# Performance work log

Measured on AMD Instinct MI355X. Metric: run time of the kernel, lower is better.

## Reference

```python
import jax, jax.numpy as jnp
import numpy as np

NUM_POINTS = 32
POINT_DIM = 4
HIDDEN_DIM = 256
BATCH = 8192


def setup_inputs() -> dict:
    key = jax.random.key(0)
    k1, k2, k3 = jax.random.split(key, 3)
    path_data = jax.random.normal(k1, (BATCH, NUM_POINTS * POINT_DIM), dtype=jnp.float32)
    # per-step Linear(point_dim+hidden_dim -> hidden_dim); torch Linear weight layout [out, in]
    fan_in = POINT_DIM + HIDDEN_DIM
    scale = 1.0 / np.sqrt(fan_in)
    W = jax.random.uniform(k2, (NUM_POINTS, HIDDEN_DIM, fan_in), dtype=jnp.float32, minval=-scale, maxval=scale)
    b = jax.random.uniform(k3, (NUM_POINTS, HIDDEN_DIM), dtype=jnp.float32, minval=-scale, maxval=scale)
    return {"path_data": path_data, "W": W, "b": b}


def reference(path_data, W, b):
    P, H = W.shape[0], W.shape[1]
    B = path_data.shape[0]
    pd = W.shape[2] - H
    # chunks: [P, B, point_dim]
    chunks = path_data.reshape(B, P, pd).transpose(1, 0, 2)

    def step(h, xs):
        wp, Wi, bi = xs
        # concat order matches torch: (curr_hidden, current_wp)
        combined = jnp.concatenate([h, wp], axis=1)  # [B, H+pd]
        h_new = jax.nn.relu(combined @ Wi.T + bi)    # [B, H]
        return h_new, h_new

    h0 = jnp.zeros((B, H), dtype=path_data.dtype)
    _, feats = jax.lax.scan(step, h0, (chunks, W, b))  # feats: [P, B, H]
    return feats.transpose(1, 0, 2).reshape(B, P * H)
```

## Files before the change

### kernel.cpp

```cpp
#include <hip/hip_runtime.h>

typedef __attribute__((ext_vector_type(8))) short bf16x8;
typedef __attribute__((ext_vector_type(16))) float f32x16;

#define NPTS 32
#define HID 256
#define FANIN 260
#define NKB 17
#define OUTSTRIDE 8192

__device__ __forceinline__ unsigned short f2bf(float f) {
  unsigned u = __builtin_bit_cast(unsigned, f);
  u += 0x7fffu + ((u >> 16) & 1u);
  return (unsigned short)(u >> 16);
}

__global__ __launch_bounds__(256) void prep_kernel(
    const float* __restrict__ W, const float* __restrict__ bias,
    bf16x8* __restrict__ pack) {
  int tid = blockIdx.x * 256 + threadIdx.x;
  int lane = tid & 63;
  int kb = (tid >> 6) % NKB;
  int rest = (tid >> 6) / NKB;
  int ct = rest & 7;
  int p = rest >> 3;
  if (p >= NPTS) return;
  int n = ct * 32 + (lane & 31);
  int g = lane >> 5;
  const float* wrow = W + (size_t)(p * HID + n) * FANIN;
  unsigned short e[8];
  if (kb < 16) {
    int k0 = kb * 16 + g * 8;
#pragma unroll
    for (int i = 0; i < 8; ++i) e[i] = f2bf(wrow[k0 + i]);
  } else {
#pragma unroll
    for (int i = 0; i < 8; ++i) e[i] = 0;
    if (g == 0) {
      e[0] = f2bf(wrow[256]);
      e[1] = f2bf(wrow[257]);
      e[2] = f2bf(wrow[258]);
      e[3] = f2bf(wrow[259]);
      e[4] = f2bf(bias[p * HID + n]);
    }
  }
  bf16x8 v;
#pragma unroll
  for (int i = 0; i < 8; ++i) v[i] = (short)e[i];
  pack[tid] = v;
}

__global__ __launch_bounds__(512, 1) void enc_kernel(
    const float* __restrict__ path, const bf16x8* __restrict__ pack,
    float* __restrict__ out) {
  __shared__ __align__(16) char lds[32768];
  const int tid = threadIdx.x;
  const int lane = tid & 63;
  const int w = tid >> 6;
  const int col = lane & 31;
  const int g = lane >> 5;
  const int b0 = blockIdx.x * 32;

  {
    int4 z = make_int4(0, 0, 0, 0);
    *reinterpret_cast<int4*>(lds + tid * 32) = z;
    *reinterpret_cast<int4*>(lds + tid * 32 + 16) = z;
  }
  __syncthreads();

  const float4* prow =
      reinterpret_cast<const float4*>(path + (size_t)(b0 + col) * 128);

  int cur = 0;
  const int swz = col << 4;

  for (int p = 0; p < NPTS; ++p) {
    const bf16x8* Bp = pack + (size_t)((p * 8 + w) * NKB) * 64 + lane;

    f32x16 acc0, acc1;
#pragma unroll
    for (int i = 0; i < 16; ++i) { acc0[i] = 0.0f; acc1[i] = 0.0f; }

    float4 px = prow[p];
    bf16x8 ax;
#pragma unroll
    for (int i = 0; i < 8; ++i) ax[i] = 0;
    if (g == 0) {
      ax[0] = (short)f2bf(px.x);
      ax[1] = (short)f2bf(px.y);
      ax[2] = (short)f2bf(px.z);
      ax[3] = (short)f2bf(px.w);
      ax[4] = (short)0x3F80;
    }

    const char* hb = lds + cur * 16384;
#pragma unroll
    for (int kb = 0; kb < 16; ++kb) {
      bf16x8 a = *reinterpret_cast<const bf16x8*>(
          hb + col * 512 + ((kb * 32 + g * 16) ^ swz));
      bf16x8 bb = Bp[kb * 64];
      if (kb & 1)
        acc1 = __builtin_amdgcn_mfma_f32_32x32x16_bf16(a, bb, acc1, 0, 0, 0);
      else
        acc0 = __builtin_amdgcn_mfma_f32_32x32x16_bf16(a, bb, acc0, 0, 0, 0);
    }
    acc0 = __builtin_amdgcn_mfma_f32_32x32x16_bf16(ax, Bp[16 * 64], acc0, 0, 0, 0);

    char* hn = lds + (cur ^ 1) * 16384;
    float* outp = out + (size_t)b0 * OUTSTRIDE + p * 256 + w * 32 + col;
#pragma unroll
    for (int r = 0; r < 16; ++r) {
      int rr = (r & 3) + 8 * (r >> 2) + 4 * g;
      float v = fmaxf(acc0[r] + acc1[r], 0.0f);
      outp[(size_t)rr * OUTSTRIDE] = v;
      *reinterpret_cast<unsigned short*>(
          hn + rr * 512 + (((w * 32 + col) * 2) ^ (rr << 4))) = f2bf(v);
    }
    __syncthreads();
    cur ^= 1;
  }
}

extern "C" void kernel_launch(void* const* d_in, const int* in_sizes, int n_in,
                              void* d_out, int out_size, void* d_ws,
                              size_t ws_size, hipStream_t stream) {
  const float* path = (const float*)d_in[0];
  const float* W = (const float*)d_in[1];
  const float* bias = (const float*)d_in[2];
  float* out = (float*)d_out;
  bf16x8* pack = (bf16x8*)d_ws;

  prep_kernel<<<1088, 256, 0, stream>>>(W, bias, pack);
  enc_kernel<<<256, 512, 0, stream>>>(path, pack, out);
}
```

Measured before the change: 100.7 us.

## Prefetch next step's weights into registers and use lighter barriers in encoder

Loads all weight fragments for the next recurrence step into a second register set (ping-pong BA/BB) while the current step's MFMAs run, and also prefetches the next point's input. It replaces __syncthreads with an LDS-only waitcnt plus s_barrier so global stores need not drain at each step. Output stores become nontemporal, and the launch bound is raised to two blocks per CU. The risks are higher register pressure from two full weight sets, possible spills under the new occupancy hint, and one redundant prefetch of step 0 on the last iteration.

```diff
diff --git a/kernel.cpp b/kernel.cpp
--- a/kernel.cpp
+++ b/kernel.cpp
@@ -50,7 +50,7 @@
   pack[tid] = v;
 }
 
-__global__ __launch_bounds__(512, 1) void enc_kernel(
+__global__ __launch_bounds__(512, 2) void enc_kernel(
     const float* __restrict__ path, const bf16x8* __restrict__ pack,
     float* __restrict__ out) {
   __shared__ __align__(16) char lds[32768];
@@ -66,59 +66,78 @@
     *reinterpret_cast<int4*>(lds + tid * 32) = z;
     *reinterpret_cast<int4*>(lds + tid * 32 + 16) = z;
   }
-  __syncthreads();
 
   const float4* prow =
       reinterpret_cast<const float4*>(path + (size_t)(b0 + col) * 128);
+  float* outbase = out + (size_t)b0 * OUTSTRIDE;
+  const int swz = col << 4;
+  int cur = 0;
 
-  int cur = 0;
-  const int swz = col << 4;
+  bf16x8 BA[NKB], BB[NKB];
+  float4 pxA, pxB;
+  {
+    const bf16x8* Bp0 = pack + (size_t)w * NKB * 64 + lane;
+#pragma unroll
+    for (int kb = 0; kb < NKB; ++kb) BA[kb] = Bp0[kb * 64];
+    pxA = prow[0];
+  }
+  __syncthreads();
 
-  for (int p = 0; p < NPTS; ++p) {
-    const bf16x8* Bp = pack + (size_t)((p * 8 + w) * NKB) * 64 + lane;
+#define STEP(P, BC, BN, PX, PXN, PNEXT)                                       \
+  {                                                                           \
+    const int p_ = (P);                                                       \
+    const bf16x8* Bnp =                                                       \
+        pack + ((size_t)((PNEXT) * 8 + w) * NKB) * 64 + lane;                 \
+    f32x16 acc0, acc1;                                                        \
+    _Pragma("unroll") for (int i = 0; i < 16; ++i) {                          \
+      acc0[i] = 0.0f;                                                         \
+      acc1[i] = 0.0f;                                                         \
+    }                                                                         \
+    bf16x8 ax;                                                                \
+    _Pragma("unroll") for (int i = 0; i < 8; ++i) ax[i] = 0;                  \
+    if (g == 0) {                                                             \
+      ax[0] = (short)f2bf((PX).x);                                            \
+      ax[1] = (short)f2bf((PX).y);                                            \
+      ax[2] = (short)f2bf((PX).z);                                            \
+      ax[3] = (short)f2bf((PX).w);                                            \
+      ax[4] = (short)0x3F80;                \
+    }                                                                         \
+    const char* hb = lds + cur * 16384;                                       \
+    _Pragma("unroll") for (int kb = 0; kb < 16; ++kb) {                       \
+      bf16x8 a = *reinterpret_cast<const bf16x8*>(                            \
+          hb + col * 512 + ((kb * 32 + g * 16) ^ swz));                       \
+      if (kb & 1)                                                             \
+        acc1 = __builtin_amdgcn_mfma_f32_32x32x16_bf16(a, (BC)[kb], acc1,     \
+                                                       0, 0, 0);              \
+      else                                                                    \
+        acc0 = __builtin_amdgcn_mfma_f32_32x32x16_bf16(a, (BC)[kb], acc0,     \
+                                                       0, 0, 0);              \
+      (BN)[kb] = Bnp[kb * 64]; \
+    }                                                                         \
+    acc0 = __builtin_amdgcn_mfma_f32_32x32x16_bf16(ax, (BC)[16], acc0,        \
+                                                   0, 0, 0);                  \
+    (BN)[16] = Bnp[16 * 64];                                                  \
+    (PXN) = prow[(PNEXT)];                                                    \
+    char* hn = lds + (cur ^ 1) * 16384;                                       \
+    float* outp = outbase + p_ * 256 + w * 32 + col;                          \
+    _Pragma("unroll") for (int r = 0; r < 16; ++r) {                          \
+      int rr = (r & 3) + 8 * (r >> 2) + 4 * g;        \
+      float v = fmaxf(acc0[r] + acc1[r], 0.0f);                               \
+      __builtin_nontemporal_store(v, outp + (size_t)rr * OUTSTRIDE);          \
+      *reinterpret_cast<unsigned short*>(                                     \
+          hn + rr * 512 + (((w * 32 + col) * 2) ^ (rr << 4))) = f2bf(v);      \
+    }                                                                         \
+    asm volatile("s_waitcnt lgkmcnt(0)" ::: "memory");                        \
+    __builtin_amdgcn_s_barrier();                                             \
+    cur ^= 1;                                                                 \
+  }
 
-    f32x16 acc0, acc1;
-#pragma unroll
-    for (int i = 0; i < 16; ++i) { acc0[i] = 0.0f; acc1[i] = 0.0f; }
-
-    float4 px = prow[p];
-    bf16x8 ax;
-#pragma unroll
-    for (int i = 0; i < 8; ++i) ax[i] = 0;
-    if (g == 0) {
-      ax[0] = (short)f2bf(px.x);
-      ax[1] = (short)f2bf(px.y);
-      ax[2] = (short)f2bf(px.z);
-      ax[3] = (short)f2bf(px.w);
-      ax[4] = (short)0x3F80;
-    }
-
-    const char* hb = lds + cur * 16384;
-#pragma unroll
-    for (int kb = 0; kb < 16; ++kb) {
-      bf16x8 a = *reinterpret_cast<const bf16x8*>(
-          hb + col * 512 + ((kb * 32 + g * 16) ^ swz));
-      bf16x8 bb = Bp[kb * 64];
-      if (kb & 1)
-        acc1 = __builtin_amdgcn_mfma_f32_32x32x16_bf16(a, bb, acc1, 0, 0, 0);
-      else
-        acc0 = __builtin_amdgcn_mfma_f32_32x32x16_bf16(a, bb, acc0, 0, 0, 0);
-    }
-    acc0 = __builtin_amdgcn_mfma_f32_32x32x16_bf16(ax, Bp[16 * 64], acc0, 0, 0, 0);
-
-    char* hn = lds + (cur ^ 1) * 16384;
-    float* outp = out + (size_t)b0 * OUTSTRIDE + p * 256 + w * 32 + col;
-#pragma unroll
-    for (int r = 0; r < 16; ++r) {
-      int rr = (r & 3) + 8 * (r >> 2) + 4 * g;
-      float v = fmaxf(acc0[r] + acc1[r], 0.0f);
-      outp[(size_t)rr * OUTSTRIDE] = v;
-      *reinterpret_cast<unsigned short*>(
-          hn + rr * 512 + (((w * 32 + col) * 2) ^ (rr << 4))) = f2bf(v);
-    }
-    __syncthreads();
-    cur ^= 1;
+  for (int p = 0; p < NPTS; p += 2) {
+    const int pn2 = (p + 2 < NPTS) ? (p + 2) : 0;
+    STEP(p, BA, BB, pxA, pxB, (p + 1));
+    STEP((p + 1), BB, BA, pxB, pxA, pn2);
   }
+#undef STEP
 }
 
 extern "C" void kernel_launch(void* const* d_in, const int* in_sizes, int n_in,
```

Result: faster. 93.54 us (-7.1%).

## Warp-specialize encoder with store waves and register-prefetched weights

Applied to the files above, without the earlier changes.

The encoder block gains two extra waves that stream each step's output from a double-buffered LDS staging area to global memory with nontemporal 16-byte stores. This takes the strided scalar global stores off the MFMA waves. The compute waves keep the next step's packed weight fragments in registers, prefetched during the current step's MFMAs, to hide global load latency. The prep kernel now stages W rows through LDS for coalesced reads. The cost is higher register and LDS use (96KB LDS per block) and a raw s_barrier handshake between producer and consumer waves.

```diff
diff --git a/kernel.cpp b/kernel.cpp
--- a/kernel.cpp
+++ b/kernel.cpp
@@ -2,6 +2,7 @@
 
 typedef __attribute__((ext_vector_type(8))) short bf16x8;
 typedef __attribute__((ext_vector_type(16))) float f32x16;
+typedef __attribute__((ext_vector_type(4))) float f32x4;
 
 #define NPTS 32
 #define HID 256
@@ -18,106 +19,133 @@
 __global__ __launch_bounds__(256) void prep_kernel(
     const float* __restrict__ W, const float* __restrict__ bias,
     bf16x8* __restrict__ pack) {
-  int tid = blockIdx.x * 256 + threadIdx.x;
-  int lane = tid & 63;
-  int kb = (tid >> 6) % NKB;
-  int rest = (tid >> 6) / NKB;
-  int ct = rest & 7;
-  int p = rest >> 3;
-  if (p >= NPTS) return;
-  int n = ct * 32 + (lane & 31);
-  int g = lane >> 5;
-  const float* wrow = W + (size_t)(p * HID + n) * FANIN;
-  unsigned short e[8];
-  if (kb < 16) {
-    int k0 = kb * 16 + g * 8;
-#pragma unroll
-    for (int i = 0; i < 8; ++i) e[i] = f2bf(wrow[k0 + i]);
-  } else {
+  __shared__ float wl[32 * FANIN];
+  const int p = blockIdx.x >> 3;
+  const int nb = blockIdx.x & 7;
+  const int t = threadIdx.x;
+  const f32x4* src = reinterpret_cast<const f32x4*>(
+      W + ((size_t)p * HID + nb * 32) * FANIN);
+  for (int i = t; i < 32 * FANIN / 4; i += 256)
+    *reinterpret_cast<f32x4*>(wl + i * 4) = src[i];
+  __syncthreads();
+  const int lane = t & 63;
+  const int wv = t >> 6;
+  const int col = lane & 31;
+  const int g = lane >> 5;
+  const float* rowp = wl + col * FANIN;
+  for (int kb = wv; kb < NKB; kb += 4) {
+    unsigned short e[8];
 #pragma unroll
     for (int i = 0; i < 8; ++i) e[i] = 0;
-    if (g == 0) {
-      e[0] = f2bf(wrow[256]);
-      e[1] = f2bf(wrow[257]);
-      e[2] = f2bf(wrow[258]);
-      e[3] = f2bf(wrow[259]);
-      e[4] = f2bf(bias[p * HID + n]);
+    if (kb < 16) {
+      int k0 = kb * 16 + g * 8;
+#pragma unroll
+      for (int i = 0; i < 8; ++i) e[i] = f2bf(rowp[k0 + i]);
+    } else if (g == 0) {
+      e[0] = f2bf(rowp[256]);
+      e[1] = f2bf(rowp[257]);
+      e[2] = f2bf(rowp[258]);
+      e[3] = f2bf(rowp[259]);
+      e[4] = f2bf(bias[p * HID + nb * 32 + col]);
     }
+    bf16x8 v;
+#pragma unroll
+    for (int i = 0; i < 8; ++i) v[i] = (short)e[i];
+    pack[(((size_t)p * 8 + nb) * NKB + kb) * 64 + lane] = v;
   }
-  bf16x8 v;
-#pragma unroll
-  for (int i = 0; i < 8; ++i) v[i] = (short)e[i];
-  pack[tid] = v;
 }
 
-__global__ __launch_bounds__(512, 1) void enc_kernel(
+__global__ __launch_bounds__(640, 3) void enc_kernel(
     const float* __restrict__ path, const bf16x8* __restrict__ pack,
     float* __restrict__ out) {
-  __shared__ __align__(16) char lds[32768];
+  __shared__ __align__(16) char lds[98304];
   const int tid = threadIdx.x;
   const int lane = tid & 63;
   const int w = tid >> 6;
-  const int col = lane & 31;
-  const int g = lane >> 5;
   const int b0 = blockIdx.x * 32;
 
-  {
-    int4 z = make_int4(0, 0, 0, 0);
-    *reinterpret_cast<int4*>(lds + tid * 32) = z;
-    *reinterpret_cast<int4*>(lds + tid * 32 + 16) = z;
+  if (tid < 512) {
+    f32x4 z = {0.0f, 0.0f, 0.0f, 0.0f};
+    *reinterpret_cast<f32x4*>(lds + tid * 32) = z;
+    *reinterpret_cast<f32x4*>(lds + tid * 32 + 16) = z;
   }
   __syncthreads();
 
-  const float4* prow =
-      reinterpret_cast<const float4*>(path + (size_t)(b0 + col) * 128);
+  if (w < 8) {
+    const int col = lane & 31;
+    const int g = lane >> 5;
+    const int swz = col << 4;
+    const float4* prow =
+        reinterpret_cast<const float4*>(path + (size_t)(b0 + col) * 128);
+    bf16x8 BC[NKB];
+    {
+      const bf16x8* Bp0 = pack + (size_t)w * NKB * 64 + lane;
+#pragma unroll
+      for (int kb = 0; kb < NKB; ++kb) BC[kb] = Bp0[kb * 64];
+    }
+    for (int p = 0; p < NPTS; ++p) {
+      const int pn = (p + 1 < NPTS) ? p + 1 : 0;
+      const bf16x8* Bnp = pack + ((size_t)(pn * 8 + w) * NKB) * 64 + lane;
+      float4 px = prow[p];
+      f32x16 acc0, acc1;
+#pragma unroll
+      for (int i = 0; i < 16; ++i) {
+        acc0[i] = 0.0f;
+        acc1[i] = 0.0f;
+      }
+      const char* hb = lds + (p & 1) * 16384;
+#pragma unroll
+      for (int kb = 0; kb < 16; ++kb) {
+        bf16x8 a = *reinterpret_cast<const bf16x8*>(
+            hb + col * 512 + ((kb * 32 + g * 16) ^ swz));
+        if (kb & 1)
+          acc1 = __builtin_amdgcn_mfma_f32_32x32x16_bf16(a, BC[kb], acc1, 0, 0, 0);
+        else
+          acc0 = __builtin_amdgcn_mfma_f32_32x32x16_bf16(a, BC[kb], acc0, 0, 0, 0);
+        BC[kb] = Bnp[kb * 64];
+      }
+      bf16x8 ax;
+#pragma unroll
+      for (int i = 0; i < 8; ++i) ax[i] = 0;
+      if (g == 0) {
+        ax[0] = (short)f2bf(px.x);
+        ax[1] = (short)f2bf(px.y);
+        ax[2] = (short)f2bf(px.z);
+        ax[3] = (short)f2bf(px.w);
+        ax[4] = (short)0x3F80;
+      }
+      acc0 = __builtin_amdgcn_mfma_f32_32x32x16_bf16(ax, BC[16], acc0, 0, 0, 0);
+      BC[16] = Bnp[16 * 64];
 
-  int cur = 0;
-  const int swz = col << 4;
-
-  for (int p = 0; p < NPTS; ++p) {
-    const bf16x8* Bp = pack + (size_t)((p * 8 + w) * NKB) * 64 + lane;
-
-    f32x16 acc0, acc1;
+      char* hn = lds + ((p + 1) & 1) * 16384;
+      float* os = reinterpret_cast<float*>(lds + 32768 + (p & 1) * 32768);
 #pragma unroll
-    for (int i = 0; i < 16; ++i) { acc0[i] = 0.0f; acc1[i] = 0.0f; }
-
-    float4 px = prow[p];
-    bf16x8 ax;
+      for (int r = 0; r < 16; ++r) {
+        int rr = (r & 3) + 8 * (r >> 2) + 4 * g;
+        float v = fmaxf(acc0[r] + acc1[r], 0.0f);
+        os[rr * 256 + w * 32 + col] = v;
+        *reinterpret_cast<unsigned short*>(
+            hn + rr * 512 + (((w * 32 + col) * 2) ^ (rr << 4))) = f2bf(v);
+      }
+      asm volatile("s_waitcnt lgkmcnt(0)" ::: "memory");
+      __builtin_amdgcn_s_barrier();
+    }
+  } else {
+    const int sid = w - 8;
+    float* outbase = out + (size_t)b0 * OUTSTRIDE;
+    for (int p = 0; p < NPTS; ++p) {
+      __builtin_amdgcn_s_barrier();
+      const f32x4* os =
+          reinterpret_cast<const f32x4*>(lds + 32768 + (p & 1) * 32768);
+      float* ob = outbase + p * 256;
 #pragma unroll
-    for (int i = 0; i < 8; ++i) ax[i] = 0;
-    if (g == 0) {
-      ax[0] = (short)f2bf(px.x);
-      ax[1] = (short)f2bf(px.y);
-      ax[2] = (short)f2bf(px.z);
-      ax[3] = (short)f2bf(px.w);
-      ax[4] = (short)0x3F80;
+      for (int r = 0; r < 16; ++r) {
+        int row = sid * 16 + r;
+        f32x4 v = os[row * 64 + lane];
+        __builtin_nontemporal_store(
+            v, reinterpret_cast<f32x4*>(ob + (size_t)row * OUTSTRIDE) + lane);
+      }
     }
-
-    const char* hb = lds + cur * 16384;
-#pragma unroll
-    for (int kb = 0; kb < 16; ++kb) {
-      bf16x8 a = *reinterpret_cast<const bf16x8*>(
-          hb + col * 512 + ((kb * 32 + g * 16) ^ swz));
-      bf16x8 bb = Bp[kb * 64];
-      if (kb & 1)
-        acc1 = __builtin_amdgcn_mfma_f32_32x32x16_bf16(a, bb, acc1, 0, 0, 0);
-      else
-        acc0 = __builtin_amdgcn_mfma_f32_32x32x16_bf16(a, bb, acc0, 0, 0, 0);
-    }
-    acc0 = __builtin_amdgcn_mfma_f32_32x32x16_bf16(ax, Bp[16 * 64], acc0, 0, 0, 0);
-
-    char* hn = lds + (cur ^ 1) * 16384;
-    float* outp = out + (size_t)b0 * OUTSTRIDE + p * 256 + w * 32 + col;
-#pragma unroll
-    for (int r = 0; r < 16; ++r) {
-      int rr = (r & 3) + 8 * (r >> 2) + 4 * g;
-      float v = fmaxf(acc0[r] + acc1[r], 0.0f);
-      outp[(size_t)rr * OUTSTRIDE] = v;
-      *reinterpret_cast<unsigned short*>(
-          hn + rr * 512 + (((w * 32 + col) * 2) ^ (rr << 4))) = f2bf(v);
-    }
-    __syncthreads();
-    cur ^= 1;
   }
 }
 
@@ -130,6 +158,6 @@
   float* out = (float*)d_out;
   bf16x8* pack = (bf16x8*)d_ws;
 
-  prep_kernel<<<1088, 256, 0, stream>>>(W, bias, pack);
-  enc_kernel<<<256, 512, 0, stream>>>(path, pack, out);
+  prep_kernel<<<256, 256, 0, stream>>>(W, bias, pack);
+  enc_kernel<<<256, 640, 0, stream>>>(path, pack, out);
 }
```

Result: slower. 120.7 us (+19.9%).
